# Kernel optimization log

Hardware: AMD Instinct MI355X
Metric: run time of the kernel (lower is better)

Reference implementation:

```python
import jax, jax.numpy as jnp
import numpy as np

NUM_HEADS = 8

def _gelu(x):
    return jax.nn.gelu(x, approximate=False)

def _ln(x, w, b, eps=1e-5):
    m = x.mean(-1, keepdims=True)
    v = ((x - m) ** 2).mean(-1, keepdims=True)
    return (x - m) / jnp.sqrt(v + eps) * w + b

def _conv(x, w, pad):
    return jax.lax.conv_general_dilated(x, w, (1, 1), [(pad, pad), (pad, pad)],
                                        dimension_numbers=('NCHW', 'OIHW', 'NCHW'))

def _dwconv(x, w):
    return jax.lax.conv_general_dilated(x, w, (1, 1), [(1, 1), (1, 1)],
                                        feature_group_count=x.shape[1],
                                        dimension_numbers=('NCHW', 'OIHW', 'NCHW'))

def setup_inputs():
    B, T, N, C, K = 4, 3, 4096, 256, 100
    ks = jax.random.split(jax.random.key(0), 16)
    p = lambda i, shape: (0.02 * jax.random.normal(ks[i], shape)).astype(jnp.float32)
    z = lambda n: jnp.zeros((n,), jnp.float32)
    return {
        'x': jax.random.normal(ks[0], (B, N, C), jnp.float32),
        'mem': jax.random.normal(ks[1], (B * T, N, C), jnp.float32),
        'conv1_w': p(2, (C, C, 7, 7)), 'conv1_b': z(C),
        'conv2_w': p(3, (C, C, 1, 1)), 'conv2_b': z(C),
        'conv3_w': p(4, (K, C, 1, 1)),
        'sim_alpha': jnp.ones((1,), jnp.float32), 'sim_beta': jnp.zeros((1,), jnp.float32),
        'ln_w': jnp.ones((C,), jnp.float32), 'ln_b': z(C),
        'q_w': p(5, (C, C)), 'q_b': z(C),
        'k_w': p(6, (C, C)), 'k_b': z(C),
        'v_w': p(7, (C, C)), 'v_b': z(C),
        'proj_w': p(8, (C, C)), 'proj_b': z(C),
        'fc1_w': p(9, (4 * C, C)), 'fc1_b': z(4 * C),
        'dw_w': p(10, (4 * C, 1, 3, 3)), 'dw_b': z(4 * C),
        'fc2_w': p(11, (C, 4 * C)), 'fc2_b': z(C),
        'H': 64, 'W': 64, 't': 3,
    }

def reference(x, mem, conv1_w, conv1_b, conv2_w, conv2_b, conv3_w, sim_alpha, sim_beta,
              ln_w, ln_b, q_w, q_b, k_w, k_b, v_w, v_b, proj_w, proj_b,
              fc1_w, fc1_b, dw_w, dw_b, fc2_w, fc2_b, H, W, t):
    B, N, C = x.shape
    T = t + 1
    # stack memory frames with current frame: [B, T, N, C]
    xt = jnp.concatenate([mem.reshape(B, t, N, C), x[:, None]], axis=1)
    img = xt.reshape(B * T, N, C).transpose(0, 2, 1).reshape(B * T, C, H, W)
    h = _gelu(_conv(img, conv1_w, 3) + conv1_b[:, None, None])
    h = _gelu(_conv(h, conv2_w, 0) + conv2_b[:, None, None])
    cz = _conv(h, conv3_w, 0)                      # [B*T, K, H, W]
    K = cz.shape[1]
    center = jax.nn.softmax(cz.reshape(B, T, K, N), axis=-1)
    center = jnp.einsum('btkn,btnc->btkc', center, xt)  # cluster centers [B,T,K,C]
    last, prev = center[:, -1], center[:, :-1]
    num = jnp.einsum('bkc,bskc->bsk', last, prev)
    den = jnp.maximum(jnp.linalg.norm(last, axis=-1)[:, None] * jnp.linalg.norm(prev, axis=-1), 1e-8)
    cos = jax.nn.sigmoid(sim_beta + sim_alpha * (num / den))  # [B, T-1, K]
    C_in = last + (cos[..., None] * prev).sum(axis=1)
    C_in = _ln(C_in, ln_w, ln_b)
    # cross-attention: queries = current frame tokens, keys/values = centers
    hd = C // NUM_HEADS
    q = (x @ q_w.T + q_b).reshape(B, N, NUM_HEADS, hd) * (hd ** -0.5)
    k = (C_in @ k_w.T + k_b).reshape(B, K, NUM_HEADS, hd)
    v = (C_in @ v_w.T + v_b).reshape(B, K, NUM_HEADS, hd)
    attn = jax.nn.softmax(jnp.einsum('bnhd,bkhd->bhnk', q, k), axis=-1)
    o = jnp.einsum('bhnk,bkhd->bnhd', attn, v).reshape(B, N, C)
    o = o @ proj_w.T + proj_b
    out = x + _ln(o, ln_w, ln_b)
    # MLP with depthwise conv
    y = out @ fc1_w.T + fc1_b                      # [B, N, 4C]
    yi = y.transpose(0, 2, 1).reshape(B, 4 * C, H, W)
    yi = _dwconv(yi, dw_w) + dw_b[:, None, None]
    y = _gelu(yi.reshape(B, 4 * C, N).transpose(0, 2, 1))
    y = y @ fc2_w.T + fc2_b
    return out + _ln(y, ln_w, ln_b)
```

## Files before the change

### kernel.cpp

```cpp
#include <hip/hip_runtime.h>
#include <math.h>

#define NN 4096
#define CC 256
#define HH 64
#define BT 16
#define KCC 100
#define NHH 8
#define HDD 32
#define C4 1024

typedef unsigned short bf16_t;
typedef short s16x8 __attribute__((ext_vector_type(8)));
typedef float f32x4 __attribute__((ext_vector_type(4)));
typedef float f32x16 __attribute__((ext_vector_type(16)));

__device__ __forceinline__ float bf2f(bf16_t h) {
  return __uint_as_float(((unsigned)h) << 16);
}
__device__ __forceinline__ bf16_t f2bf(float f) {
  unsigned u = __float_as_uint(f);
  return (bf16_t)((u + 0x7FFFu + ((u >> 16) & 1u)) >> 16);
}

__device__ __forceinline__ float gelu_f(float x) {
  return 0.5f * x * (1.0f + erff(x * 0.7071067811865475f));
}

__device__ __forceinline__ void g2l16(const void* g, void* l) {
  __builtin_amdgcn_global_load_lds((const __attribute__((address_space(1))) void*)g,
                                   (__attribute__((address_space(3))) void*)l, 16, 0, 0);
}

__device__ __forceinline__ float block_sum256(float v) {
  __shared__ float sh[4];
#pragma unroll
  for (int off = 32; off; off >>= 1) v += __shfl_xor(v, off, 64);
  __syncthreads();
  if ((threadIdx.x & 63) == 0) sh[threadIdx.x >> 6] = v;
  __syncthreads();
  return sh[0] + sh[1] + sh[2] + sh[3];
}

__device__ __forceinline__ const float* xt_base(const float* x, const float* mem, int bt) {
  int b = bt >> 2, tt = bt & 3;
  return (tt < 3) ? (mem + (size_t)(b * 3 + tt) * NN * CC)
                  : (x + (size_t)b * NN * CC);
}

__global__ __launch_bounds__(256) void prologue(const float* __restrict__ x,
                                                const float* __restrict__ mem,
                                                bf16_t* __restrict__ xtb,
                                                const float* __restrict__ w1,
                                                bf16_t* __restrict__ wtb,
                                                const float* __restrict__ c2w,
                                                const float* __restrict__ c3w,
                                                const float* __restrict__ qw,
                                                const float* __restrict__ pw,
                                                const float* __restrict__ f1w,
                                                const float* __restrict__ f2w,
                                                bf16_t* __restrict__ wbz) {
  int bid = blockIdx.x;
  int tid = threadIdx.x;
  if (bid < 16384) {
    int i = bid * 256 + tid;
    int c4 = i & 63;
    int n = (i >> 6) & 4095;
    int bt = i >> 18;
    const float* src = xt_base(x, mem, bt) + (size_t)n * CC + c4 * 4;
    float4 v = *(const float4*)src;
    ushort4 o;
    o.x = f2bf(v.x); o.y = f2bf(v.y); o.z = f2bf(v.z); o.w = f2bf(v.w);
    *(ushort4*)(xtb + (size_t)i * 4) = o;
  } else if (bid < 19520) {
    int i = (bid - 16384) * 256 + tid;
    int cj = i & 7;
    int t = i >> 3;
    int co = t & 63; t >>= 6;
    int oc = t & 3; t >>= 2;
    int kx = t % 7; t /= 7;
    int cq = t & 3; t >>= 2;
    int cg = t & 7;
    int ky = t >> 3;
    int ci = cg * 32 + oc * 8 + cj;
    int cog = cq * 64 + co;
    wtb[i] = f2bf(w1[((size_t)(cog * CC + ci) * 7 + ky) * 7 + kx]);
  } else {
    int j = (bid - 19520) * 256 + tid;
    float v;
    if (j < 65536) v = c2w[j];
    else if (j < 91136) v = c3w[j - 65536];
    else if (j < 156672) v = qw[j - 91136];
    else if (j < 222208) v = pw[j - 156672];
    else if (j < 484352) v = f1w[j - 222208];
    else v = f2w[j - 484352];
    wbz[j] = f2bf(v);
  }
}

__global__ __launch_bounds__(1024, 4) void conv1_mfma(const bf16_t* __restrict__ xtb,
                                                      const bf16_t* __restrict__ wtb,
                                                      const float* __restrict__ bias,
                                                      bf16_t* __restrict__ h1) {
  int bid = blockIdx.x;
  int cq = bid & 3;
  int rem = bid >> 2;
  int bt = rem & 15;
  int rb = rem >> 4;
  int r0 = rb * 16;
  int co0 = cq * 64;
  int tid = threadIdx.x;
  int wv = tid >> 6;
  int lane = tid & 63;
  int l31 = lane & 31;
  int h = lane >> 5;
  __shared__ __align__(16) short As[22][4][70][8];
  __shared__ __align__(16) short Ws[2][7][4][64][8];
  {
    s16x8 z = {0, 0, 0, 0, 0, 0, 0, 0};
    for (int i = tid; i < 22 * 4 * 70; i += 1024) *(s16x8*)((short*)As + i * 8) = z;
  }
  __syncthreads();
  f32x16 acc[2][2] = {};
  const bf16_t* xb = xtb + (size_t)bt * (NN * CC);
  for (int cig = 0; cig < 8; ++cig) {
    int ci0 = cig * 32;
    for (int t = wv; t < 88; t += 16) {
      int rr = t >> 2, go = t & 3;
      int r = r0 - 3 + rr;
      if (r >= 0 && r < HH) {
        const bf16_t* gsrc = xb + ((size_t)(r * 64 + lane)) * CC + ci0 + go * 8;
        g2l16(gsrc, &As[rr][go][3][0]);
      }
    }
    {
      const bf16_t* wk = wtb + ((size_t)((0 * 8 + cig) * 4 + cq)) * (1792 * 8);
      for (int t = wv; t < 28; t += 16)
        g2l16(wk + (size_t)t * 512 + lane * 8, (short*)Ws[0] + t * 512);
    }
    __syncthreads();
    for (int ky = 0; ky < 7; ++ky) {
      int cur = ky & 1;
      if (ky < 6) {
        const bf16_t* wk = wtb + ((size_t)(((ky + 1) * 8 + cig) * 4 + cq)) * (1792 * 8);
        for (int t = wv; t < 28; t += 16)
          g2l16(wk + (size_t)t * 512 + lane * 8, (short*)Ws[cur ^ 1] + t * 512);
      }
#pragma unroll
      for (int kx = 0; kx < 7; ++kx) {
        s16x8 fa[2][2], fb[2][2];
#pragma unroll
        for (int mt = 0; mt < 2; ++mt)
#pragma unroll
          for (int ks = 0; ks < 2; ++ks) {
            fa[mt][ks] = *(const s16x8*)&As[wv + ky][ks * 2 + h][mt * 32 + l31 + kx][0];
            fb[mt][ks] = *(const s16x8*)&Ws[cur][kx][ks * 2 + h][mt * 32 + l31][0];
          }
#pragma unroll
        for (int ks = 0; ks < 2; ++ks)
#pragma unroll
          for (int mt = 0; mt < 2; ++mt)
#pragma unroll
            for (int nt = 0; nt < 2; ++nt)
              acc[mt][nt] = __builtin_amdgcn_mfma_f32_32x32x16_bf16(
                  fa[mt][ks], fb[nt][ks], acc[mt][nt], 0, 0, 0);
      }
      __syncthreads();
    }
  }
  int row = r0 + wv;
  const size_t xbase = (size_t)bt * (NN * CC);
#pragma unroll
  for (int nt = 0; nt < 2; ++nt) {
    int co = co0 + nt * 32 + l31;
    float bs = bias[co];
#pragma unroll
    for (int mt = 0; mt < 2; ++mt) {
#pragma unroll
      for (int rg = 0; rg < 16; ++rg) {
        int px = mt * 32 + (rg & 3) + 8 * (rg >> 2) + 4 * h;
        float vv = acc[mt][nt][rg] + bs;
        h1[xbase + (size_t)(row * 64 + px) * CC + co] = f2bf(gelu_f(vv));
      }
    }
  }
}

template <int GELU, int BIAS, int TOUT, int OBF>
__global__ __launch_bounds__(256) void gemm_mfma(const bf16_t* __restrict__ A,
                                                 const bf16_t* __restrict__ W,
                                                 const float* __restrict__ bias,
                                                 void* __restrict__ outp,
                                                 int M, int N, int K, int ldo,
                                                 size_t aStr, size_t oStr) {
  __shared__ short As[128][72];
  __shared__ short Bs[128][72];
  A += (size_t)blockIdx.z * aStr;
  size_t obase = (size_t)blockIdx.z * oStr;
  int tid = threadIdx.x;
  int n0 = blockIdx.x * 128, m0 = blockIdx.y * 128;
  int lane = tid & 63, wv = tid >> 6;
  int wm = wv & 1, wn = wv >> 1;
  int lm = lane & 15, g = lane >> 4;
  f32x4 acc[4][4] = {};
  int r1 = tid >> 2, kq = tid & 3;
  int r2 = r1 + 64;
  for (int k0 = 0; k0 < K; k0 += 64) {
    *(s16x8*)&As[r1][kq * 8] = *(const s16x8*)(A + (size_t)(m0 + r1) * K + k0 + kq * 8);
    *(s16x8*)&As[r1][32 + kq * 8] =
        *(const s16x8*)(A + (size_t)(m0 + r1) * K + k0 + 32 + kq * 8);
    *(s16x8*)&As[r2][kq * 8] = *(const s16x8*)(A + (size_t)(m0 + r2) * K + k0 + kq * 8);
    *(s16x8*)&As[r2][32 + kq * 8] =
        *(const s16x8*)(A + (size_t)(m0 + r2) * K + k0 + 32 + kq * 8);
    s16x8 z = {0, 0, 0, 0, 0, 0, 0, 0};
    s16x8 b1 = z, b2 = z, b3 = z, b4 = z;
    if (n0 + r1 < N) {
      b1 = *(const s16x8*)(W + (size_t)(n0 + r1) * K + k0 + kq * 8);
      b2 = *(const s16x8*)(W + (size_t)(n0 + r1) * K + k0 + 32 + kq * 8);
    }
    if (n0 + r2 < N) {
      b3 = *(const s16x8*)(W + (size_t)(n0 + r2) * K + k0 + kq * 8);
      b4 = *(const s16x8*)(W + (size_t)(n0 + r2) * K + k0 + 32 + kq * 8);
    }
    *(s16x8*)&Bs[r1][kq * 8] = b1;
    *(s16x8*)&Bs[r1][32 + kq * 8] = b2;
    *(s16x8*)&Bs[r2][kq * 8] = b3;
    *(s16x8*)&Bs[r2][32 + kq * 8] = b4;
    __syncthreads();
#pragma unroll
    for (int ks = 0; ks < 2; ++ks) {
      s16x8 af[4], bf[4];
#pragma unroll
      for (int mt = 0; mt < 4; ++mt)
        af[mt] = *(const s16x8*)&As[wm * 64 + mt * 16 + lm][ks * 32 + g * 8];
#pragma unroll
      for (int nt = 0; nt < 4; ++nt)
        bf[nt] = *(const s16x8*)&Bs[wn * 64 + nt * 16 + lm][ks * 32 + g * 8];
#pragma unroll
      for (int mt = 0; mt < 4; ++mt)
#pragma unroll
        for (int nt = 0; nt < 4; ++nt)
          acc[mt][nt] = __builtin_amdgcn_mfma_f32_16x16x32_bf16(af[mt], bf[nt],
                                                                acc[mt][nt], 0, 0, 0);
    }
    __syncthreads();
  }
#pragma unroll
  for (int nt = 0; nt < 4; ++nt) {
    int n = n0 + wn * 64 + nt * 16 + lm;
    if (n >= N) continue;
    float bs = BIAS ? bias[n] : 0.f;
#pragma unroll
    for (int mt = 0; mt < 4; ++mt) {
#pragma unroll
      for (int rg = 0; rg < 4; ++rg) {
        int m = m0 + wm * 64 + mt * 16 + g * 4 + rg;
        float v = acc[mt][nt][rg] + bs;
        if (GELU) v = gelu_f(v);
        size_t idx = obase + (TOUT ? ((size_t)n * ldo + m) : ((size_t)m * ldo + n));
        if (OBF)
          ((bf16_t*)outp)[idx] = f2bf(v);
        else
          ((float*)outp)[idx] = v;
      }
    }
  }
}

__global__ __launch_bounds__(256) void gemm_kv(const float* __restrict__ cin,
                                               const float* __restrict__ kw,
                                               const float* __restrict__ kbias,
                                               const float* __restrict__ vw,
                                               const float* __restrict__ vbias,
                                               float* __restrict__ kout,
                                               float* __restrict__ vout) {
  const float* Wm = blockIdx.z ? vw : kw;
  const float* bias = blockIdx.z ? vbias : kbias;
  float* outp = blockIdx.z ? vout : kout;
  const int M = 400, N = 256, K = 256;
  __shared__ float As[16][68];
  __shared__ float Ws[16][68];
  int tid = threadIdx.x;
  int n0 = blockIdx.x * 64, m0 = blockIdx.y * 64;
  int txn = tid & 15, tym = tid >> 4;
  int mi = tid >> 2, kq = (tid & 3) * 4;
  float acc[4][4] = {};
  for (int k0 = 0; k0 < K; k0 += 16) {
    float4 av = {0, 0, 0, 0}, wvv = {0, 0, 0, 0};
    if (m0 + mi < M) av = *(const float4*)&cin[(size_t)(m0 + mi) * K + k0 + kq];
    if (n0 + mi < N) wvv = *(const float4*)&Wm[(size_t)(n0 + mi) * K + k0 + kq];
    As[kq + 0][mi] = av.x; As[kq + 1][mi] = av.y; As[kq + 2][mi] = av.z; As[kq + 3][mi] = av.w;
    Ws[kq + 0][mi] = wvv.x; Ws[kq + 1][mi] = wvv.y; Ws[kq + 2][mi] = wvv.z; Ws[kq + 3][mi] = wvv.w;
    __syncthreads();
#pragma unroll
    for (int ki = 0; ki < 16; ++ki) {
      float4 a4 = *(const float4*)&As[ki][tym * 4];
      float4 w4 = *(const float4*)&Ws[ki][txn * 4];
      float am[4] = {a4.x, a4.y, a4.z, a4.w};
      float wn[4] = {w4.x, w4.y, w4.z, w4.w};
#pragma unroll
      for (int i = 0; i < 4; ++i)
#pragma unroll
        for (int j = 0; j < 4; ++j) acc[i][j] += am[i] * wn[j];
    }
    __syncthreads();
  }
#pragma unroll
  for (int i = 0; i < 4; ++i) {
    int m = m0 + tym * 4 + i;
    if (m >= M) continue;
#pragma unroll
    for (int j = 0; j < 4; ++j) {
      int n = n0 + txn * 4 + j;
      outp[(size_t)m * 256 + n] = acc[i][j] + bias[n];
    }
  }
}

__global__ __launch_bounds__(256) void softmax_rows(bf16_t* __restrict__ p) {
  __shared__ float sh[8];
  int tid = threadIdx.x;
  bf16_t* base = p + (size_t)blockIdx.x * NN + tid * 16;
  s16x8 a = *(const s16x8*)base;
  s16x8 b = *(const s16x8*)(base + 8);
  float vals[16];
#pragma unroll
  for (int j = 0; j < 8; ++j) {
    vals[j] = bf2f((bf16_t)a[j]);
    vals[8 + j] = bf2f((bf16_t)b[j]);
  }
  float mx = -1e30f;
#pragma unroll
  for (int j = 0; j < 16; ++j) mx = fmaxf(mx, vals[j]);
#pragma unroll
  for (int off = 32; off; off >>= 1) mx = fmaxf(mx, __shfl_xor(mx, off, 64));
  if ((tid & 63) == 0) sh[tid >> 6] = mx;
  __syncthreads();
  mx = fmaxf(fmaxf(sh[0], sh[1]), fmaxf(sh[2], sh[3]));
  float s = 0.f;
#pragma unroll
  for (int j = 0; j < 16; ++j) {
    vals[j] = expf(vals[j] - mx);
    s += vals[j];
  }
#pragma unroll
  for (int off = 32; off; off >>= 1) s += __shfl_xor(s, off, 64);
  if ((tid & 63) == 0) sh[4 + (tid >> 6)] = s;
  __syncthreads();
  s = sh[4] + sh[5] + sh[6] + sh[7];
  float inv = 1.f / s;
  s16x8 oa, ob;
#pragma unroll
  for (int j = 0; j < 8; ++j) {
    oa[j] = (short)f2bf(vals[j] * inv);
    ob[j] = (short)f2bf(vals[8 + j] * inv);
  }
  *(s16x8*)base = oa;
  *(s16x8*)(base + 8) = ob;
}

__global__ __launch_bounds__(256) void center_mfma(const bf16_t* __restrict__ soft,
                                                   const bf16_t* __restrict__ xtb,
                                                   float* __restrict__ partial) {
  int c0 = blockIdx.x * 128;
  int bt = blockIdx.y;
  int nc = blockIdx.z;
  int tid = threadIdx.x;
  int lane = tid & 63, wv = tid >> 6;
  int wm = wv & 1, wn = wv >> 1;
  int lm = lane & 15, g = lane >> 4;
  __shared__ short As[128][40];
  __shared__ short Bs[128][40];
  f32x4 acc[4][4] = {};
  int r1 = tid >> 2, kq = tid & 3;
  int r2 = r1 + 64;
  int bk = tid & 31, bc = (tid >> 5) * 16;
  const bf16_t* sb = soft + (size_t)bt * NN + (size_t)nc * 512;
  const bf16_t* xb = xtb + ((size_t)bt * NN + (size_t)nc * 512) * CC + c0;
  for (int k0 = 0; k0 < 512; k0 += 32) {
    *(s16x8*)&As[r1][kq * 8] =
        *(const s16x8*)(sb + (size_t)r1 * (BT * NN) + k0 + kq * 8);
    if (r2 < KCC)
      *(s16x8*)&As[r2][kq * 8] =
          *(const s16x8*)(sb + (size_t)r2 * (BT * NN) + k0 + kq * 8);
    s16x8 v0 = *(const s16x8*)(xb + (size_t)(k0 + bk) * CC + bc);
    s16x8 v1 = *(const s16x8*)(xb + (size_t)(k0 + bk) * CC + bc + 8);
#pragma unroll
    for (int j = 0; j < 8; ++j) Bs[bc + j][bk] = v0[j];
#pragma unroll
    for (int j = 0; j < 8; ++j) Bs[bc + 8 + j][bk] = v1[j];
    __syncthreads();
    s16x8 af[4], bf[4];
#pragma unroll
    for (int mt = 0; mt < 4; ++mt)
      af[mt] = *(const s16x8*)&As[wm * 64 + mt * 16 + lm][g * 8];
#pragma unroll
    for (int nt = 0; nt < 4; ++nt)
      bf[nt] = *(const s16x8*)&Bs[wn * 64 + nt * 16 + lm][g * 8];
#pragma unroll
    for (int mt = 0; mt < 4; ++mt)
#pragma unroll
      for (int nt = 0; nt < 4; ++nt)
        acc[mt][nt] = __builtin_amdgcn_mfma_f32_16x16x32_bf16(af[mt], bf[nt],
                                                              acc[mt][nt], 0, 0, 0);
    __syncthreads();
  }
  size_t obase = ((size_t)nc * BT + bt) * (KCC * CC);
#pragma unroll
  for (int nt = 0; nt < 4; ++nt) {
    int c = c0 + wn * 64 + nt * 16 + lm;
#pragma unroll
    for (int mt = 0; mt < 4; ++mt) {
#pragma unroll
      for (int rg = 0; rg < 4; ++rg) {
        int m = wm * 64 + mt * 16 + g * 4 + rg;
        if (m < KCC) partial[obase + (size_t)m * CC + c] = acc[mt][nt][rg];
      }
    }
  }
}

__global__ __launch_bounds__(256) void sim_cin(const float* __restrict__ partial,
                                               const float* __restrict__ alpha_p,
                                               const float* __restrict__ beta_p,
                                               const float* __restrict__ lnw,
                                               const float* __restrict__ lnb,
                                               float* __restrict__ cin) {
  int b = blockIdx.x / KCC, kc = blockIdx.x % KCC;
  int c = threadIdx.x;
  float p0 = 0.f, p1 = 0.f, p2 = 0.f, lst = 0.f;
#pragma unroll
  for (int nc = 0; nc < 8; ++nc) {
    size_t base = ((size_t)nc * BT) * KCC * CC;
    p0 += partial[base + ((size_t)(b * 4 + 0) * KCC + kc) * CC + c];
    p1 += partial[base + ((size_t)(b * 4 + 1) * KCC + kc) * CC + c];
    p2 += partial[base + ((size_t)(b * 4 + 2) * KCC + kc) * CC + c];
    lst += partial[base + ((size_t)(b * 4 + 3) * KCC + kc) * CC + c];
  }
  float ll = block_sum256(lst * lst);
  float q0 = block_sum256(p0 * p0);
  float q1 = block_sum256(p1 * p1);
  float q2 = block_sum256(p2 * p2);
  float d0 = block_sum256(lst * p0);
  float d1 = block_sum256(lst * p1);
  float d2 = block_sum256(lst * p2);
  float alpha = alpha_p[0], beta = beta_p[0];
  float nl = sqrtf(ll);
  float c0 = 1.f / (1.f + expf(-(beta + alpha * (d0 / fmaxf(nl * sqrtf(q0), 1e-8f)))));
  float c1 = 1.f / (1.f + expf(-(beta + alpha * (d1 / fmaxf(nl * sqrtf(q1), 1e-8f)))));
  float c2 = 1.f / (1.f + expf(-(beta + alpha * (d2 / fmaxf(nl * sqrtf(q2), 1e-8f)))));
  float v = lst + c0 * p0 + c1 * p1 + c2 * p2;
  float m = block_sum256(v) * (1.f / CC);
  float dv = v - m;
  float var = block_sum256(dv * dv) * (1.f / CC);
  cin[((size_t)b * KCC + kc) * CC + c] = dv * rsqrtf(var + 1e-5f) * lnw[c] + lnb[c];
}

__global__ __launch_bounds__(256) void attn2(const float* __restrict__ q,
                                             const float* __restrict__ kb,
                                             const float* __restrict__ vb,
                                             bf16_t* __restrict__ ob) {
  int b = blockIdx.y;
  int n0 = blockIdx.x * 8;
  int tid = threadIdx.x;
  __shared__ float qs[8][256];
  __shared__ float Ks[32][257];
  __shared__ float sc[8][8][104];
#pragma unroll
  for (int r = 0; r < 8; ++r)
    qs[r][tid] = q[((size_t)b * NN + n0 + r) * CC + tid] * 0.17677669529663687f;
  int nn = tid >> 5, kcl = tid & 31;
  for (int kt = 0; kt < 4; ++kt) {
    int kbase = kt * 32;
    int rows = (kbase + 32 <= KCC) ? 32 : (KCC - kbase);
    __syncthreads();
    for (int idx = tid; idx < rows * 256; idx += 256) {
      int rr = idx >> 8, cc = idx & 255;
      Ks[rr][cc] = kb[((size_t)b * KCC + kbase + rr) * CC + cc];
    }
    __syncthreads();
    if (kcl < rows) {
#pragma unroll
      for (int h = 0; h < NHH; ++h) {
        float s = 0.f;
#pragma unroll
        for (int d = 0; d < HDD; ++d) s += qs[nn][h * HDD + d] * Ks[kcl][h * HDD + d];
        sc[nn][h][kbase + kcl] = s;
      }
    }
  }
  __syncthreads();
  {
    int tnn = tid >> 5, th = (tid >> 2) & 7, j = tid & 3;
    float mx = -1e30f;
    for (int kc = j * 25; kc < j * 25 + 25; ++kc) mx = fmaxf(mx, sc[tnn][th][kc]);
    mx = fmaxf(mx, __shfl_xor(mx, 1, 64));
    mx = fmaxf(mx, __shfl_xor(mx, 2, 64));
    float sm = 0.f;
    for (int kc = j * 25; kc < j * 25 + 25; ++kc) {
      float e = expf(sc[tnn][th][kc] - mx);
      sc[tnn][th][kc] = e;
      sm += e;
    }
    sm += __shfl_xor(sm, 1, 64);
    sm += __shfl_xor(sm, 2, 64);
    float inv = 1.f / sm;
    for (int kc = j * 25; kc < j * 25 + 25; ++kc) sc[tnn][th][kc] *= inv;
  }
  __syncthreads();
  float o[8] = {0, 0, 0, 0, 0, 0, 0, 0};
  int h = tid >> 5;
  for (int kc = 0; kc < KCC; ++kc) {
    float v = vb[((size_t)b * KCC + kc) * CC + tid];
#pragma unroll
    for (int r = 0; r < 8; ++r) o[r] += sc[r][h][kc] * v;
  }
#pragma unroll
  for (int r = 0; r < 8; ++r)
    ob[((size_t)b * NN + n0 + r) * CC + tid] = f2bf(o[r]);
}

template <int WB>
__global__ __launch_bounds__(256) void add_ln(const float* __restrict__ res,
                                              const float* __restrict__ y,
                                              const float* __restrict__ lnw,
                                              const float* __restrict__ lnb,
                                              float* __restrict__ dst,
                                              bf16_t* __restrict__ dst_b) {
  size_t row = (size_t)blockIdx.x * 4 + (threadIdx.x >> 6);
  int lane = threadIdx.x & 63;
  int c = lane * 4;
  float4 v = *(const float4*)&y[row * CC + c];
  float s = v.x + v.y + v.z + v.w;
#pragma unroll
  for (int off = 32; off; off >>= 1) s += __shfl_xor(s, off, 64);
  float m = s * (1.f / CC);
  float d0 = v.x - m, d1 = v.y - m, d2 = v.z - m, d3 = v.w - m;
  float q = d0 * d0 + d1 * d1 + d2 * d2 + d3 * d3;
#pragma unroll
  for (int off = 32; off; off >>= 1) q += __shfl_xor(q, off, 64);
  float inv = rsqrtf(q * (1.f / CC) + 1e-5f);
  float4 r4 = *(const float4*)&res[row * CC + c];
  float4 lw = *(const float4*)&lnw[c];
  float4 lb = *(const float4*)&lnb[c];
  float4 o;
  o.x = r4.x + d0 * inv * lw.x + lb.x;
  o.y = r4.y + d1 * inv * lw.y + lb.y;
  o.z = r4.z + d2 * inv * lw.z + lb.z;
  o.w = r4.w + d3 * inv * lw.w + lb.w;
  *(float4*)&dst[row * CC + c] = o;
  if (WB) {
    ushort4 ob;
    ob.x = f2bf(o.x); ob.y = f2bf(o.y); ob.z = f2bf(o.z); ob.w = f2bf(o.w);
    *(ushort4*)&dst_b[row * CC + c] = ob;
  }
}

__global__ __launch_bounds__(256) void dwconv_kernel(const bf16_t* __restrict__ y1,
                                                     const float* __restrict__ dww,
                                                     const float* __restrict__ dwb,
                                                     bf16_t* __restrict__ y2) {
  int b = blockIdx.x >> 12;
  int n = blockIdx.x & 4095;
  int h = n >> 6, w = n & 63;
  int c40 = threadIdx.x * 4;
  float wreg[4][9];
#pragma unroll
  for (int j = 0; j < 4; ++j)
#pragma unroll
    for (int t2 = 0; t2 < 9; ++t2) wreg[j][t2] = dww[(size_t)(c40 + j) * 9 + t2];
  float acc[4] = {0, 0, 0, 0};
#pragma unroll
  for (int dy = 0; dy < 3; ++dy) {
    int r = h + dy - 1;
    if (r < 0 || r >= HH) continue;
#pragma unroll
    for (int dx = 0; dx < 3; ++dx) {
      int cl = w + dx - 1;
      if (cl < 0 || cl >= 64) continue;
      ushort4 u = *(const ushort4*)(y1 + ((size_t)b * NN + r * 64 + cl) * C4 + c40);
      int t2 = dy * 3 + dx;
      acc[0] += bf2f(u.x) * wreg[0][t2];
      acc[1] += bf2f(u.y) * wreg[1][t2];
      acc[2] += bf2f(u.z) * wreg[2][t2];
      acc[3] += bf2f(u.w) * wreg[3][t2];
    }
  }
  ushort4 o;
  o.x = f2bf(gelu_f(acc[0] + dwb[c40 + 0]));
  o.y = f2bf(gelu_f(acc[1] + dwb[c40 + 1]));
  o.z = f2bf(gelu_f(acc[2] + dwb[c40 + 2]));
  o.w = f2bf(gelu_f(acc[3] + dwb[c40 + 3]));
  *(ushort4*)(y2 + ((size_t)b * NN + n) * C4 + c40) = o;
}

extern "C" void kernel_launch(void* const* d_in, const int* in_sizes, int n_in,
                              void* d_out, int out_size, void* d_ws, size_t ws_size,
                              hipStream_t stream) {
  const float* x = (const float*)d_in[0];
  const float* mem = (const float*)d_in[1];
  const float* conv1_w = (const float*)d_in[2];
  const float* conv1_b = (const float*)d_in[3];
  const float* conv2_w = (const float*)d_in[4];
  const float* conv2_b = (const float*)d_in[5];
  const float* conv3_w = (const float*)d_in[6];
  const float* sim_a = (const float*)d_in[7];
  const float* sim_b = (const float*)d_in[8];
  const float* ln_w = (const float*)d_in[9];
  const float* ln_b = (const float*)d_in[10];
  const float* q_w = (const float*)d_in[11];
  const float* q_b = (const float*)d_in[12];
  const float* k_w = (const float*)d_in[13];
  const float* k_b = (const float*)d_in[14];
  const float* v_w = (const float*)d_in[15];
  const float* v_b = (const float*)d_in[16];
  const float* proj_w = (const float*)d_in[17];
  const float* proj_b = (const float*)d_in[18];
  const float* fc1_w = (const float*)d_in[19];
  const float* fc1_b = (const float*)d_in[20];
  const float* dw_w = (const float*)d_in[21];
  const float* dw_b = (const float*)d_in[22];
  const float* fc2_w = (const float*)d_in[23];
  const float* fc2_b = (const float*)d_in[24];

  char* base = (char*)d_ws;
  bf16_t* xtb = (bf16_t*)(base);
  bf16_t* by1 = (bf16_t*)(base);
  bf16_t* bh1 = (bf16_t*)(base + 33554432);
  float* qb = (float*)(base + 33554432);
  float* outb = (float*)(base + 33554432);
  float* partial = (float*)(base + 50331648);
  float* pbuf = (float*)(base + 50331648);
  bf16_t* y2 = (bf16_t*)(base + 50331648);
  bf16_t* czt = (bf16_t*)(base + 67108864);
  bf16_t* obz = (bf16_t*)(base + 67108864);
  bf16_t* outb_b = (bf16_t*)(base + 67108864);
  bf16_t* wtb = (bf16_t*)(base + 80216064);
  bf16_t* h2c = (bf16_t*)(base + 80216064);
  bf16_t* wbz = (bf16_t*)(base + 96993280);
  float* cin = (float*)(base + 100124672);
  float* kb = (float*)(base + 100534272);
  float* vb = (float*)(base + 100943872);
  float* dout = (float*)d_out;

  bf16_t* conv2_wb = wbz;
  bf16_t* conv3_wb = wbz + 65536;
  bf16_t* q_wb = wbz + 91136;
  bf16_t* proj_wb = wbz + 156672;
  bf16_t* fc1_wb = wbz + 222208;
  bf16_t* fc2_wb = wbz + 484352;

  prologue<<<22436, 256, 0, stream>>>(x, mem, xtb, conv1_w, wtb, conv2_w, conv3_w,
                                      q_w, proj_w, fc1_w, fc2_w, wbz);
  conv1_mfma<<<256, 1024, 0, stream>>>(xtb, wtb, conv1_b, bh1);
  for (int i = 0; i < 2; ++i) {
    gemm_mfma<1, 1, 0, 1><<<dim3(2, 256, 1), 256, 0, stream>>>(
        bh1 + (size_t)i * 32768 * CC, conv2_wb, conv2_b, h2c, 32768, 256, 256, 256, 0, 0);
    gemm_mfma<0, 0, 1, 1><<<dim3(1, 256, 1), 256, 0, stream>>>(
        h2c, conv3_wb, nullptr, czt + (size_t)i * 32768, 32768, 100, 256, 65536, 0, 0);
  }
  softmax_rows<<<1600, 256, 0, stream>>>(czt);
  center_mfma<<<dim3(2, 16, 8), 256, 0, stream>>>(czt, xtb, partial);
  sim_cin<<<400, 256, 0, stream>>>(partial, sim_a, sim_b, ln_w, ln_b, cin);
  gemm_mfma<0, 1, 0, 0><<<dim3(2, 32, 4), 256, 0, stream>>>(
      xtb + (size_t)3 * NN * CC, q_wb, q_b, qb, 4096, 256, 256, 256,
      (size_t)4 * NN * CC, (size_t)NN * CC);
  gemm_kv<<<dim3(4, 7, 2), 256, 0, stream>>>(cin, k_w, k_b, v_w, v_b, kb, vb);
  attn2<<<dim3(512, 4), 256, 0, stream>>>(qb, kb, vb, obz);
  gemm_mfma<0, 1, 0, 0><<<dim3(2, 128, 1), 256, 0, stream>>>(obz, proj_wb, proj_b, pbuf,
                                                             16384, 256, 256, 256, 0, 0);
  add_ln<1><<<4096, 256, 0, stream>>>(x, pbuf, ln_w, ln_b, outb, outb_b);
  gemm_mfma<0, 1, 0, 1><<<dim3(8, 128, 1), 256, 0, stream>>>(outb_b, fc1_wb, fc1_b, by1,
                                                             16384, 1024, 256, 1024, 0, 0);
  dwconv_kernel<<<16384, 256, 0, stream>>>(by1, dw_w, dw_b, y2);
  gemm_mfma<0, 1, 0, 0><<<dim3(2, 32, 4), 256, 0, stream>>>(
      y2, fc2_wb, fc2_b, dout, 4096, 256, 1024, 256,
      (size_t)NN * C4, (size_t)NN * CC);
  add_ln<0><<<4096, 256, 0, stream>>>(outb, dout, ln_w, ln_b, dout, nullptr);
}
```

Measured before the change: 824.8 us.

## Fuse conv2 and conv3 1x1 GEMMs into one kernel keeping h2 in LDS

Replaces the two-chunk loop of separate conv2 (bias+GELU) and conv3 GEMM launches with a single 512-thread kernel. Each block computes a 128-row conv2 tile, stores the GELU output in shared memory, then multiplies by the conv3 weights and writes the transposed center logits. This removes the global write and re-read of the intermediate h2 buffer and three extra launches. It also merges the seven block reductions in sim_cin into one shuffle and shared-memory pass. The trade-off is about 124 KB of LDS per block, which limits each CU to one block with no load/compute overlap. The conv3 pass also reads padded weight rows past the 112-row staging buffer, though those results are masked out.

Result: faster. 804.8 us (-2.4%).

```diff
diff --git a/kernel.cpp b/kernel.cpp
--- a/kernel.cpp
+++ b/kernel.cpp
@@ -186,6 +186,116 @@
   }
 }
 
+__global__ __launch_bounds__(512) void conv23(const bf16_t* __restrict__ bh1,
+                                              const bf16_t* __restrict__ w2,
+                                              const float* __restrict__ b2,
+                                              const bf16_t* __restrict__ w3,
+                                              bf16_t* __restrict__ czt) {
+  __shared__ __align__(16) char smem[126720];
+  short (*As2)[72] = (short(*)[72])smem;
+  short (*Bs2)[72] = (short(*)[72])(smem + 18432);
+  short (*h2s)[264] = (short(*)[264])smem;
+  short (*w3s)[264] = (short(*)[264])(smem + 67584);
+  short (*ot)[132] = (short(*)[132])smem;
+  int tid = threadIdx.x;
+  int m0 = blockIdx.x * 128;
+  int lane = tid & 63, wv = tid >> 6;
+  int wm = wv & 1, wn = wv >> 1;
+  int lm = lane & 15, g = lane >> 4;
+  f32x4 acc[4][4] = {};
+  int r1 = tid >> 2, kq = tid & 3;
+  int br = tid >> 1, bq = (tid & 1) * 32;
+  for (int k0 = 0; k0 < 256; k0 += 64) {
+    *(s16x8*)&As2[r1][kq * 8] =
+        *(const s16x8*)(bh1 + (size_t)(m0 + r1) * 256 + k0 + kq * 8);
+    *(s16x8*)&As2[r1][32 + kq * 8] =
+        *(const s16x8*)(bh1 + (size_t)(m0 + r1) * 256 + k0 + 32 + kq * 8);
+#pragma unroll
+    for (int j = 0; j < 4; ++j)
+      *(s16x8*)&Bs2[br][bq + j * 8] =
+          *(const s16x8*)(w2 + (size_t)br * 256 + k0 + bq + j * 8);
+    __syncthreads();
+#pragma unroll
+    for (int ks = 0; ks < 2; ++ks) {
+      s16x8 af[4], bf[4];
+#pragma unroll
+      for (int mt = 0; mt < 4; ++mt)
+        af[mt] = *(const s16x8*)&As2[wm * 64 + mt * 16 + lm][ks * 32 + g * 8];
+#pragma unroll
+      for (int nt = 0; nt < 4; ++nt)
+        bf[nt] = *(const s16x8*)&Bs2[wn * 64 + nt * 16 + lm][ks * 32 + g * 8];
+#pragma unroll
+      for (int mt = 0; mt < 4; ++mt)
+#pragma unroll
+        for (int nt = 0; nt < 4; ++nt)
+          acc[mt][nt] = __builtin_amdgcn_mfma_f32_16x16x32_bf16(af[mt], bf[nt],
+                                                                acc[mt][nt], 0, 0, 0);
+    }
+    __syncthreads();
+  }
+#pragma unroll
+  for (int nt = 0; nt < 4; ++nt) {
+    int c = wn * 64 + nt * 16 + lm;
+    float bs = b2[c];
+#pragma unroll
+    for (int mt = 0; mt < 4; ++mt) {
+#pragma unroll
+      for (int rg = 0; rg < 4; ++rg) {
+        int m = wm * 64 + mt * 16 + g * 4 + rg;
+        h2s[m][c] = (short)f2bf(gelu_f(acc[mt][nt][rg] + bs));
+      }
+    }
+  }
+  {
+    s16x8 z = {0, 0, 0, 0, 0, 0, 0, 0};
+    for (int t = tid; t < 112 * 32; t += 512) {
+      int rr = t >> 5, cc = (t & 31) * 8;
+      s16x8 vv = z;
+      if (rr < 100) vv = *(const s16x8*)(w3 + (size_t)rr * 256 + cc);
+      *(s16x8*)&w3s[rr][cc] = vv;
+    }
+  }
+  __syncthreads();
+  f32x4 acc3[4][2] = {};
+  int n_base = wn * 32;
+#pragma unroll
+  for (int k0 = 0; k0 < 256; k0 += 32) {
+    s16x8 af[4], bf[2];
+#pragma unroll
+    for (int mt = 0; mt < 4; ++mt)
+      af[mt] = *(const s16x8*)&h2s[wm * 64 + mt * 16 + lm][k0 + g * 8];
+#pragma unroll
+    for (int nt = 0; nt < 2; ++nt)
+      bf[nt] = *(const s16x8*)&w3s[n_base + nt * 16 + lm][k0 + g * 8];
+#pragma unroll
+    for (int mt = 0; mt < 4; ++mt)
+#pragma unroll
+      for (int nt = 0; nt < 2; ++nt)
+        acc3[mt][nt] = __builtin_amdgcn_mfma_f32_16x16x32_bf16(af[mt], bf[nt],
+                                                               acc3[mt][nt], 0, 0, 0);
+  }
+  __syncthreads();
+#pragma unroll
+  for (int nt = 0; nt < 2; ++nt) {
+    int kc = n_base + nt * 16 + lm;
+    if (kc < 100) {
+#pragma unroll
+      for (int mt = 0; mt < 4; ++mt) {
+#pragma unroll
+        for (int rg = 0; rg < 4; ++rg) {
+          int px = wm * 64 + mt * 16 + g * 4 + rg;
+          ot[kc][px] = (short)f2bf(acc3[mt][nt][rg]);
+        }
+      }
+    }
+  }
+  __syncthreads();
+  for (int t = tid; t < 100 * 128; t += 512) {
+    int kc = t >> 7, px = t & 127;
+    czt[(size_t)kc * 65536 + m0 + px] = (bf16_t)ot[kc][px];
+  }
+}
+
 template <int GELU, int BIAS, int TOUT, int OBF>
 __global__ __launch_bounds__(256) void gemm_mfma(const bf16_t* __restrict__ A,
                                                  const bf16_t* __restrict__ W,
@@ -437,13 +547,23 @@
     p2 += partial[base + ((size_t)(b * 4 + 2) * KCC + kc) * CC + c];
     lst += partial[base + ((size_t)(b * 4 + 3) * KCC + kc) * CC + c];
   }
-  float ll = block_sum256(lst * lst);
-  float q0 = block_sum256(p0 * p0);
-  float q1 = block_sum256(p1 * p1);
-  float q2 = block_sum256(p2 * p2);
-  float d0 = block_sum256(lst * p0);
-  float d1 = block_sum256(lst * p1);
-  float d2 = block_sum256(lst * p2);
+  float v7[7] = {lst * lst, p0 * p0, p1 * p1, p2 * p2,
+                 lst * p0, lst * p1, lst * p2};
+#pragma unroll
+  for (int off = 32; off; off >>= 1)
+#pragma unroll
+    for (int j = 0; j < 7; ++j) v7[j] += __shfl_xor(v7[j], off, 64);
+  __shared__ float sh7[4][8];
+  if ((threadIdx.x & 63) == 0)
+#pragma unroll
+    for (int j = 0; j < 7; ++j) sh7[threadIdx.x >> 6][j] = v7[j];
+  __syncthreads();
+  float s7[7];
+#pragma unroll
+  for (int j = 0; j < 7; ++j)
+    s7[j] = sh7[0][j] + sh7[1][j] + sh7[2][j] + sh7[3][j];
+  float ll = s7[0], q0 = s7[1], q1 = s7[2], q2 = s7[3];
+  float d0 = s7[4], d1 = s7[5], d2 = s7[6];
   float alpha = alpha_p[0], beta = beta_p[0];
   float nl = sqrtf(ll);
   float c0 = 1.f / (1.f + expf(-(beta + alpha * (d0 / fmaxf(nl * sqrtf(q0), 1e-8f)))));
@@ -636,7 +756,6 @@
   bf16_t* obz = (bf16_t*)(base + 67108864);
   bf16_t* outb_b = (bf16_t*)(base + 67108864);
   bf16_t* wtb = (bf16_t*)(base + 80216064);
-  bf16_t* h2c = (bf16_t*)(base + 80216064);
   bf16_t* wbz = (bf16_t*)(base + 96993280);
   float* cin = (float*)(base + 100124672);
   float* kb = (float*)(base + 100534272);
@@ -653,12 +772,7 @@
   prologue<<<22436, 256, 0, stream>>>(x, mem, xtb, conv1_w, wtb, conv2_w, conv3_w,
                                       q_w, proj_w, fc1_w, fc2_w, wbz);
   conv1_mfma<<<256, 1024, 0, stream>>>(xtb, wtb, conv1_b, bh1);
-  for (int i = 0; i < 2; ++i) {
-    gemm_mfma<1, 1, 0, 1><<<dim3(2, 256, 1), 256, 0, stream>>>(
-        bh1 + (size_t)i * 32768 * CC, conv2_wb, conv2_b, h2c, 32768, 256, 256, 256, 0, 0);
-    gemm_mfma<0, 0, 1, 1><<<dim3(1, 256, 1), 256, 0, stream>>>(
-        h2c, conv3_wb, nullptr, czt + (size_t)i * 32768, 32768, 100, 256, 65536, 0, 0);
-  }
+  conv23<<<512, 512, 0, stream>>>(bh1, conv2_wb, conv2_b, conv3_wb, czt);
   softmax_rows<<<1600, 256, 0, stream>>>(czt);
   center_mfma<<<dim3(2, 16, 8), 256, 0, stream>>>(czt, xtb, partial);
   sim_cin<<<400, 256, 0, stream>>>(partial, sim_a, sim_b, ln_w, ln_b, cin);
```
